# Kernel optimization log

Measured on AMD Instinct MI355X. Metric: run time of the kernel, lower is better.

## Reference

```python
import jax, jax.numpy as jnp
import numpy as np

N_NODES = 80000
N_EDGES = 1280000
NODE_DIM = 32
EDGE_DIM = 16
HIDDEN = 64
N_HIDDEN_LAYERS = 3  # layer_count - 1
NUM_GRAPHS = 256


def setup_inputs() -> dict:
    key = jax.random.key(0)
    ks = jax.random.split(key, 16)
    s = 0.05
    H = jax.random.normal(ks[0], (N_NODES, NODE_DIM), dtype=jnp.float32)
    Xe = jax.random.normal(ks[1], (N_EDGES, EDGE_DIM), dtype=jnp.float32)
    id_Xe = jax.random.randint(ks[2], (2, N_EDGES), 0, N_NODES, dtype=jnp.int32).astype(jnp.int64)
    batch_idx = jnp.sort(jax.random.randint(ks[3], (N_NODES,), 0, NUM_GRAPHS, dtype=jnp.int32)).astype(jnp.int64)
    # input layer: M: (node+edge)->hidden, U: (hidden+node)->hidden
    Mw0 = jax.random.normal(ks[4], (NODE_DIM + EDGE_DIM, HIDDEN), dtype=jnp.float32) * s
    Mb0 = jnp.zeros((HIDDEN,), dtype=jnp.float32)
    Uw0 = jax.random.normal(ks[5], (HIDDEN + NODE_DIM, HIDDEN), dtype=jnp.float32) * s
    Ub0 = jnp.zeros((HIDDEN,), dtype=jnp.float32)
    # hidden layers: M: (hidden+edge)->hidden, U: (2*hidden)->hidden (stacked)
    Mw_h = jax.random.normal(ks[6], (N_HIDDEN_LAYERS, HIDDEN + EDGE_DIM, HIDDEN), dtype=jnp.float32) * s
    Mb_h = jnp.zeros((N_HIDDEN_LAYERS, HIDDEN), dtype=jnp.float32)
    Uw_h = jax.random.normal(ks[7], (N_HIDDEN_LAYERS, 2 * HIDDEN, HIDDEN), dtype=jnp.float32) * s
    Ub_h = jnp.zeros((N_HIDDEN_LAYERS, HIDDEN), dtype=jnp.float32)
    # final linear head hidden -> 1
    Ww = jax.random.normal(ks[8], (HIDDEN, 1), dtype=jnp.float32) * s
    Wb = jnp.zeros((1,), dtype=jnp.float32)
    return {"H": H, "Xe": Xe, "id_Xe": id_Xe, "batch_idx": batch_idx,
            "Mw0": Mw0, "Mb0": Mb0, "Uw0": Uw0, "Ub0": Ub0,
            "Mw_h": Mw_h, "Mb_h": Mb_h, "Uw_h": Uw_h, "Ub_h": Ub_h,
            "Ww": Ww, "Wb": Wb}


def reference(H, Xe, id_Xe, batch_idx, Mw0, Mb0, Uw0, Ub0, Mw_h, Mb_h, Uw_h, Ub_h, Ww, Wb):
    n = H.shape[0]
    src = id_Xe[0]
    dst = id_Xe[1]

    def gnn_layer(h, Mw, Mb, Uw, Ub):
        # message: gather source node features, concat edge features, MLP M
        m = jax.nn.relu(jnp.concatenate([h[src], Xe], axis=-1) @ Mw + Mb)  # [E, hidden]
        # scatter-sum to target nodes
        agg = jax.ops.segment_sum(m, dst, num_segments=n)  # [N, hidden]
        # update: concat node state with aggregated message, MLP U
        return jax.nn.relu(jnp.concatenate([h, agg], axis=-1) @ Uw + Ub)

    y = gnn_layer(H, Mw0, Mb0, Uw0, Ub0)
    for i in range(Mw_h.shape[0]):
        y = gnn_layer(y, Mw_h[i], Mb_h[i], Uw_h[i], Ub_h[i])

    pooled = jax.ops.segment_sum(y, batch_idx, num_segments=NUM_GRAPHS)  # [G, hidden]
    return pooled @ Ww + Wb  # [G, 1]
```

## Files before the change

kernel.cpp:

```cpp
#include <hip/hip_runtime.h>
#include <hip/hip_fp16.h>

#define HID 64

struct alignas(8)  H4 { __half2 a, b; };
struct alignas(16) H8 { __half2 h[4]; };

typedef _Float16 h2n __attribute__((ext_vector_type(2)));

__device__ inline float dot2f(__half2 a, __half2 b, float c) {
#if __has_builtin(__builtin_amdgcn_fdot2)
    h2n an, bn;
    __builtin_memcpy(&an, &a, 4);
    __builtin_memcpy(&bn, &b, 4);
    return __builtin_amdgcn_fdot2(an, bn, c, false);
#else
    float2 af = __half22float2(a), bf = __half22float2(b);
    return c + af.x * bf.x + af.y * bf.y;
#endif
}

__global__ __launch_bounds__(256) void deg_count(const int* __restrict__ dst,
                                                 int* __restrict__ deg, int E) {
    int e = blockIdx.x * 256 + threadIdx.x;
    if (e < E) atomicAdd(&deg[dst[e]], 1);
}

__global__ __launch_bounds__(256) void scan1(const int* __restrict__ deg,
                                             int* __restrict__ rowptr,
                                             int* __restrict__ bsums, int N) {
    __shared__ int s[256];
    const int t = threadIdx.x;
    const int base = blockIdx.x * 2048 + t * 8;
    int v[8], tot = 0;
    #pragma unroll
    for (int i = 0; i < 8; i++) {
        int x = (base + i < N) ? deg[base + i] : 0;
        v[i] = tot; tot += x;
    }
    s[t] = tot; __syncthreads();
    for (int off = 1; off < 256; off <<= 1) {
        int a = (t >= off) ? s[t - off] : 0;
        __syncthreads(); s[t] += a; __syncthreads();
    }
    const int texcl = s[t] - tot;
    #pragma unroll
    for (int i = 0; i < 8; i++)
        if (base + i < N) rowptr[base + i] = texcl + v[i];
    if (t == 255) bsums[blockIdx.x] = s[255];
}

__global__ void scan2(int* bsums, int NB) {
    if (blockIdx.x == 0 && threadIdx.x == 0) {
        int run = 0;
        for (int i = 0; i < NB; i++) { int x = bsums[i]; bsums[i] = run; run += x; }
    }
}

__global__ __launch_bounds__(256) void scan3(int* __restrict__ rowptr,
                                             const int* __restrict__ bsums,
                                             int N, int E) {
    int idx = blockIdx.x * 256 + threadIdx.x;
    if (idx < N) rowptr[idx] += bsums[idx >> 11];
    if (idx == 0) rowptr[N] = E;
}

__global__ __launch_bounds__(256) void permute_k(
    const int* __restrict__ src, const int* __restrict__ dst,
    const int* __restrict__ rowptr, int* __restrict__ cursor,
    const float* __restrict__ Xe, __half* __restrict__ Xes,
    unsigned* __restrict__ pks, int E)
{
    int e = blockIdx.x * 256 + threadIdx.x;
    if (e >= E) return;
    int d = dst[e];
    int pos = rowptr[d] + atomicAdd(&cursor[d], 1);
    pks[pos] = ((unsigned)src[e] << 5) | (unsigned)(d & 31);
    const float4* xi = (const float4*)&Xe[(size_t)e * 16];
    float4 x0 = xi[0], x1 = xi[1], x2 = xi[2], x3 = xi[3];
    H8 h0, h1;
    h0.h[0] = __float22half2_rn(make_float2(x0.x, x0.y));
    h0.h[1] = __float22half2_rn(make_float2(x0.z, x0.w));
    h0.h[2] = __float22half2_rn(make_float2(x1.x, x1.y));
    h0.h[3] = __float22half2_rn(make_float2(x1.z, x1.w));
    h1.h[0] = __float22half2_rn(make_float2(x2.x, x2.y));
    h1.h[1] = __float22half2_rn(make_float2(x2.z, x2.w));
    h1.h[2] = __float22half2_rn(make_float2(x3.x, x3.y));
    h1.h[3] = __float22half2_rn(make_float2(x3.z, x3.w));
    H8* xo = (H8*)&Xes[(size_t)pos * 16];
    xo[0] = h0; xo[1] = h1;
}

template<int K1>
__global__ __launch_bounds__(256) void pm_dual(
    const float* __restrict__ Hn,
    const float* __restrict__ Wm, const float* __restrict__ bm,
    const float* __restrict__ Wu, const float* __restrict__ bu,
    __half* __restrict__ PMh, __half* __restrict__ Th, int N)
{
    constexpr int KP = K1 + 4;
    constexpr int P4 = K1 / 4;
    __shared__ float Ws[K1 * 128];
    __shared__ float Xs[32 * KP];

    const int tid = threadIdx.x;
    for (int i = tid; i < K1 * 32; i += 256) {
        const int row = i >> 5, c4 = i & 31;
        float4 v = (c4 < 16) ? *(const float4*)&Wm[row * 64 + c4 * 4]
                             : *(const float4*)&Wu[row * 64 + (c4 - 16) * 4];
        *(float4*)&Ws[row * 128 + c4 * 4] = v;
    }
    const int nbase = blockIdx.x * 32;
    for (int i = tid; i < 32 * P4; i += 256) {
        const int nl = i / P4, part = i % P4;
        const int n = nbase + nl;
        if (n < N)
            *(float4*)&Xs[nl * KP + part * 4] =
                *(const float4*)&Hn[(size_t)n * K1 + part * 4];
    }
    __syncthreads();

    const int c0 = (tid & 31) * 4;
    const int n0 = (tid >> 5) * 4;
    const float4 bv = (c0 < 64) ? *(const float4*)&bm[c0]
                                : *(const float4*)&bu[c0 - 64];

    float4 acc[4];
    #pragma unroll
    for (int i = 0; i < 4; i++) acc[i] = bv;

    #pragma unroll 4
    for (int k = 0; k < K1; k += 4) {
        const float4 w0 = *(const float4*)&Ws[(k + 0) * 128 + c0];
        const float4 w1 = *(const float4*)&Ws[(k + 1) * 128 + c0];
        const float4 w2 = *(const float4*)&Ws[(k + 2) * 128 + c0];
        const float4 w3 = *(const float4*)&Ws[(k + 3) * 128 + c0];
        #pragma unroll
        for (int ni = 0; ni < 4; ni++) {
            const float4 xv = *(const float4*)&Xs[(n0 + ni) * KP + k];
            acc[ni].x += xv.x * w0.x + xv.y * w1.x + xv.z * w2.x + xv.w * w3.x;
            acc[ni].y += xv.x * w0.y + xv.y * w1.y + xv.z * w2.y + xv.w * w3.y;
            acc[ni].z += xv.x * w0.z + xv.y * w1.z + xv.z * w2.z + xv.w * w3.z;
            acc[ni].w += xv.x * w0.w + xv.y * w1.w + xv.z * w2.w + xv.w * w3.w;
        }
    }

    #pragma unroll
    for (int ni = 0; ni < 4; ni++) {
        const int n = nbase + n0 + ni;
        if (n < N) {
            H4 o;
            o.a = __float22half2_rn(make_float2(acc[ni].x, acc[ni].y));
            o.b = __float22half2_rn(make_float2(acc[ni].z, acc[ni].w));
            if (c0 < 64) *(H4*)&PMh[(size_t)n * 64 + c0]      = o;
            else         *(H4*)&Th [(size_t)n * 64 + c0 - 64] = o;
        }
    }
}

__global__ __launch_bounds__(256) void edge_fused(
    const __half*   __restrict__ PMh,
    const __half*   __restrict__ Th,
    const __half*   __restrict__ Xes,
    const unsigned* __restrict__ pks,
    const int*      __restrict__ rowptr,
    const float*    __restrict__ Mwb,
    const float*    __restrict__ Uwb,
    float*          __restrict__ Yout,
    int N)
{
    constexpr int AGP = HID + 4;
    __shared__ float aggs[32 * AGP];

    const int tid  = threadIdx.x;
    const int wv   = tid >> 6;
    const int lane = tid & 63;
    const int c0   = (lane & 15) * 4;
    const int g    = lane >> 4;

    __half2 wh[8][4];
    #pragma unroll
    for (int p = 0; p < 8; p++)
        #pragma unroll
        for (int j = 0; j < 4; j++)
            wh[p][j] = __float22half2_rn(make_float2(Mwb[(2 * p) * 64 + c0 + j],
                                                     Mwb[(2 * p + 1) * 64 + c0 + j]));

    for (int i = tid; i < 32 * AGP; i += 256) aggs[i] = 0.f;

    const int nbase  = blockIdx.x * 32;
    const int nend   = (nbase + 32 < N) ? nbase + 32 : N;
    const int estart = rowptr[nbase];
    const int eend   = rowptr[nend];
    __syncthreads();

    int pc = estart + wv * 16;
    unsigned pk_c[4], pk_n[4], pk_n2[4];
    H4 ph_c[4], ph_n[4];
    H8 xh_c[4][2], xh_n[4][2];

    if (pc < eend) {
        #pragma unroll
        for (int s = 0; s < 4; s++) {
            const int pe = pc + g * 4 + s;
            pk_c[s] = pks[pe < eend ? pe : eend - 1];
        }
        if (pc + 64 < eend) {
            #pragma unroll
            for (int s = 0; s < 4; s++) {
                const int pe = pc + 64 + g * 4 + s;
                pk_n[s] = pks[pe < eend ? pe : eend - 1];
            }
        }
        #pragma unroll
        for (int s = 0; s < 4; s++) {
            const int pe  = pc + g * 4 + s;
            const int pcl = pe < eend ? pe : eend - 1;
            ph_c[s] = *(const H4*)&PMh[(size_t)(pk_c[s] >> 5) * 64 + c0];
            const H8* xr = (const H8*)&Xes[(size_t)pcl * 16];
            xh_c[s][0] = xr[0]; xh_c[s][1] = xr[1];
        }
    }

    for (; pc < eend; pc += 64) {
        const int pn  = pc + 64;
        const int pn2 = pc + 128;

        if (pn < eend) {
            #pragma unroll
            for (int s = 0; s < 4; s++) {
                const int pe  = pn + g * 4 + s;
                const int pcl = pe < eend ? pe : eend - 1;
                ph_n[s] = *(const H4*)&PMh[(size_t)(pk_n[s] >> 5) * 64 + c0];
                const H8* xr = (const H8*)&Xes[(size_t)pcl * 16];
                xh_n[s][0] = xr[0]; xh_n[s][1] = xr[1];
            }
        }
        if (pn2 < eend) {
            #pragma unroll
            for (int s = 0; s < 4; s++) {
                const int pe = pn2 + g * 4 + s;
                pk_n2[s] = pks[pe < eend ? pe : eend - 1];
            }
        }

        int ld_prev = -1;
        float4 racc = make_float4(0.f, 0.f, 0.f, 0.f);
        #pragma unroll
        for (int s = 0; s < 4; s++) {
            const bool valid = (pc + g * 4 + s) < eend;
            const float2 pl = __half22float2(ph_c[s].a);
            const float2 pu = __half22float2(ph_c[s].b);
            float a0 = pl.x, a1 = pl.y, a2 = pu.x, a3 = pu.y;
            #pragma unroll
            for (int p = 0; p < 8; p++) {
                const __half2 xv = xh_c[s][p >> 2].h[p & 3];
                a0 = dot2f(xv, wh[p][0], a0);
                a1 = dot2f(xv, wh[p][1], a1);
                a2 = dot2f(xv, wh[p][2], a2);
                a3 = dot2f(xv, wh[p][3], a3);
            }
            float4 v;
            v.x = fmaxf(a0, 0.f); v.y = fmaxf(a1, 0.f);
            v.z = fmaxf(a2, 0.f); v.w = fmaxf(a3, 0.f);
            const int ld = valid ? (int)(pk_c[s] & 31u) : -1;
            if (ld == ld_prev) {
                racc.x += v.x; racc.y += v.y; racc.z += v.z; racc.w += v.w;
            } else {
                if (ld_prev >= 0) {
                    float* a = &aggs[ld_prev * AGP + c0];
                    atomicAdd(a + 0, racc.x); atomicAdd(a + 1, racc.y);
                    atomicAdd(a + 2, racc.z); atomicAdd(a + 3, racc.w);
                }
                racc = v; ld_prev = ld;
            }
        }
        if (ld_prev >= 0) {
            float* a = &aggs[ld_prev * AGP + c0];
            atomicAdd(a + 0, racc.x); atomicAdd(a + 1, racc.y);
            atomicAdd(a + 2, racc.z); atomicAdd(a + 3, racc.w);
        }

        #pragma unroll
        for (int s = 0; s < 4; s++) {
            pk_c[s] = pk_n[s]; pk_n[s] = pk_n2[s];
            ph_c[s] = ph_n[s];
            xh_c[s][0] = xh_n[s][0]; xh_c[s][1] = xh_n[s][1];
        }
    }

    __syncthreads();

    {
        const int c0t = (tid & 15) * 4;
        const int r0  = tid >> 4;
        const int r1  = r0 + 16;
        const int n0g = nbase + r0, n1g = nbase + r1;
        float4 acc0 = make_float4(0.f, 0.f, 0.f, 0.f);
        float4 acc1 = make_float4(0.f, 0.f, 0.f, 0.f);
        if (n0g < N) {
            H4 th = *(const H4*)&Th[(size_t)n0g * 64 + c0t];
            float2 lo = __half22float2(th.a), hi = __half22float2(th.b);
            acc0 = make_float4(lo.x, lo.y, hi.x, hi.y);
        }
        if (n1g < N) {
            H4 th = *(const H4*)&Th[(size_t)n1g * 64 + c0t];
            float2 lo = __half22float2(th.a), hi = __half22float2(th.b);
            acc1 = make_float4(lo.x, lo.y, hi.x, hi.y);
        }
        #pragma unroll 4
        for (int k = 0; k < 64; k += 4) {
            const float4 w0 = *(const float4*)&Uwb[(k + 0) * 64 + c0t];
            const float4 w1 = *(const float4*)&Uwb[(k + 1) * 64 + c0t];
            const float4 w2 = *(const float4*)&Uwb[(k + 2) * 64 + c0t];
            const float4 w3 = *(const float4*)&Uwb[(k + 3) * 64 + c0t];
            const float4 x0 = *(const float4*)&aggs[r0 * AGP + k];
            const float4 x1 = *(const float4*)&aggs[r1 * AGP + k];
            acc0.x += x0.x * w0.x + x0.y * w1.x + x0.z * w2.x + x0.w * w3.x;
            acc0.y += x0.x * w0.y + x0.y * w1.y + x0.z * w2.y + x0.w * w3.y;
            acc0.z += x0.x * w0.z + x0.y * w1.z + x0.z * w2.z + x0.w * w3.z;
            acc0.w += x0.x * w0.w + x0.y * w1.w + x0.z * w2.w + x0.w * w3.w;
            acc1.x += x1.x * w0.x + x1.y * w1.x + x1.z * w2.x + x1.w * w3.x;
            acc1.y += x1.x * w0.y + x1.y * w1.y + x1.z * w2.y + x1.w * w3.y;
            acc1.z += x1.x * w0.z + x1.y * w1.z + x1.z * w2.z + x1.w * w3.z;
            acc1.w += x1.x * w0.w + x1.y * w1.w + x1.z * w2.w + x1.w * w3.w;
        }
        if (n0g < N) {
            float4 o;
            o.x = fmaxf(acc0.x, 0.f); o.y = fmaxf(acc0.y, 0.f);
            o.z = fmaxf(acc0.z, 0.f); o.w = fmaxf(acc0.w, 0.f);
            *(float4*)&Yout[(size_t)n0g * HID + c0t] = o;
        }
        if (n1g < N) {
            float4 o;
            o.x = fmaxf(acc1.x, 0.f); o.y = fmaxf(acc1.y, 0.f);
            o.z = fmaxf(acc1.z, 0.f); o.w = fmaxf(acc1.w, 0.f);
            *(float4*)&Yout[(size_t)n1g * HID + c0t] = o;
        }
    }
}

__global__ __launch_bounds__(256) void pool_head(
    const float* __restrict__ Y, const int* __restrict__ bidx,
    const float* __restrict__ Ww, const float* __restrict__ Wb,
    float* __restrict__ out, int N)
{
    const int g = blockIdx.x;
    int a = 0, b = N;
    while (a < b) { int m = (a + b) >> 1; if (bidx[m] < g) a = m + 1; else b = m; }
    const int lo = a;
    b = N;
    while (a < b) { int m = (a + b) >> 1; if (bidx[m] < g + 1) a = m + 1; else b = m; }
    const int hi = a;

    const int tid = threadIdx.x;
    const int c4 = tid & 15, nl = tid >> 4;
    float4 s = make_float4(0.f, 0.f, 0.f, 0.f);
    for (int n = lo + nl; n < hi; n += 16) {
        const float4 v = *(const float4*)&Y[(size_t)n * HID + c4 * 4];
        s.x += v.x; s.y += v.y; s.z += v.z; s.w += v.w;
    }
    __shared__ float red[16 * 68];
    *(float4*)&red[nl * 68 + c4 * 4] = s;
    __syncthreads();
    if (tid < 64) {
        float t = 0.f;
        #pragma unroll
        for (int r = 0; r < 16; r++) t += red[r * 68 + tid];
        t *= Ww[tid];
        #pragma unroll
        for (int off = 32; off; off >>= 1) t += __shfl_down(t, off);
        if (tid == 0) out[g] = t + Wb[0];
    }
}

extern "C" void kernel_launch(void* const* d_in, const int* in_sizes, int n_in,
                              void* d_out, int out_size, void* d_ws, size_t ws_size,
                              hipStream_t stream) {
    const float* H    = (const float*)d_in[0];
    const float* Xe   = (const float*)d_in[1];
    const int*   ids  = (const int*)d_in[2];
    const int*   bidx = (const int*)d_in[3];
    const float* Mw0  = (const float*)d_in[4];
    const float* Mb0  = (const float*)d_in[5];
    const float* Uw0  = (const float*)d_in[6];
    const float* Ub0  = (const float*)d_in[7];
    const float* MwH  = (const float*)d_in[8];
    const float* MbH  = (const float*)d_in[9];
    const float* UwH  = (const float*)d_in[10];
    const float* UbH  = (const float*)d_in[11];
    const float* Ww   = (const float*)d_in[12];
    const float* Wb   = (const float*)d_in[13];
    float* out = (float*)d_out;

    const int N = in_sizes[0] / 32;
    const int E = in_sizes[1] / 16;
    const int* src = ids;
    const int* dst = ids + E;

    float*  hbuf = (float*)d_ws;
    __half* PMh  = (__half*)(hbuf + (size_t)N * HID);
    __half* Th   = PMh + (size_t)N * HID;
    __half* Xes  = Th  + (size_t)N * HID;
    unsigned* pks = (unsigned*)(Xes + (size_t)E * 16);
    int* rowptr  = (int*)(pks + E);
    int* deg     = rowptr + (N + 1);
    int* bsums   = deg + N;

    const int NB = (N + 2047) / 2048;
    const int eblocks = (E + 255) / 256;
    const int ntile   = (N + 31) / 32;

    hipMemsetAsync(deg, 0, (size_t)N * sizeof(int), stream);
    deg_count<<<eblocks, 256, 0, stream>>>(dst, deg, E);
    scan1<<<NB, 256, 0, stream>>>(deg, rowptr, bsums, N);
    scan2<<<1, 64, 0, stream>>>(bsums, NB);
    scan3<<<(N + 255) / 256, 256, 0, stream>>>(rowptr, bsums, N, E);
    hipMemsetAsync(deg, 0, (size_t)N * sizeof(int), stream);
    permute_k<<<eblocks, 256, 0, stream>>>(src, dst, rowptr, deg,
                                           Xe, Xes, pks, E);

    pm_dual<32><<<ntile, 256, 0, stream>>>(H, Mw0, Mb0, Uw0, Ub0, PMh, Th, N);
    edge_fused<<<ntile, 256, 0, stream>>>(PMh, Th, Xes, pks, rowptr,
                                          Mw0 + 32 * HID, Uw0 + 32 * HID, hbuf, N);

    for (int l = 0; l < 3; l++) {
        const float* Mw = MwH + (size_t)l * 80 * HID;
        const float* Uw = UwH + (size_t)l * 128 * HID;
        pm_dual<64><<<ntile, 256, 0, stream>>>(hbuf, Mw, MbH + (size_t)l * HID,
                                               Uw, UbH + (size_t)l * HID, PMh, Th, N);
        edge_fused<<<ntile, 256, 0, stream>>>(PMh, Th, Xes, pks, rowptr,
                                              Mw + 64 * HID, Uw + 64 * HID, hbuf, N);
    }

    pool_head<<<256, 256, 0, stream>>>(hbuf, bidx, Ww, Wb, out, N);
}
```

Measured before the change: 967.2 us.

## Fuse next layer's node projection into edge kernel epilogue with ping-pong buffers

The edge_fused kernel is templated so that, for the first three layers, its epilogue keeps the ReLU'd node state in shared memory. It then directly computes the next layer's message and update projections (the former pm_dual work), writing them as fp16 into alternating buffers. This drops three pm_dual launches and the fp32 round trip of the hidden state through global memory. In exchange the epilogue needs an extra block sync, and each block does more register and compute work. The final layer writes fp32 output into a region that aliases the no-longer-used ping buffers.

```diff
diff --git a/kernel.cpp b/kernel.cpp
--- a/kernel.cpp
+++ b/kernel.cpp
@@ -158,6 +158,7 @@
     }
 }
 
+template<bool FUSE>
 __global__ __launch_bounds__(256) void edge_fused(
     const __half*   __restrict__ PMh,
     const __half*   __restrict__ Th,
@@ -166,6 +167,12 @@
     const int*      __restrict__ rowptr,
     const float*    __restrict__ Mwb,
     const float*    __restrict__ Uwb,
+    const float*    __restrict__ MwN,
+    const float*    __restrict__ MbN,
+    const float*    __restrict__ UwN,
+    const float*    __restrict__ UbN,
+    __half*         __restrict__ PMo,
+    __half*         __restrict__ Tho,
     float*          __restrict__ Yout,
     int N)
 {
@@ -291,51 +298,100 @@
 
     __syncthreads();
 
-    {
-        const int c0t = (tid & 15) * 4;
-        const int r0  = tid >> 4;
-        const int r1  = r0 + 16;
-        const int n0g = nbase + r0, n1g = nbase + r1;
-        float4 acc0 = make_float4(0.f, 0.f, 0.f, 0.f);
-        float4 acc1 = make_float4(0.f, 0.f, 0.f, 0.f);
-        if (n0g < N) {
-            H4 th = *(const H4*)&Th[(size_t)n0g * 64 + c0t];
-            float2 lo = __half22float2(th.a), hi = __half22float2(th.b);
-            acc0 = make_float4(lo.x, lo.y, hi.x, hi.y);
-        }
-        if (n1g < N) {
-            H4 th = *(const H4*)&Th[(size_t)n1g * 64 + c0t];
-            float2 lo = __half22float2(th.a), hi = __half22float2(th.b);
-            acc1 = make_float4(lo.x, lo.y, hi.x, hi.y);
-        }
+    const int c0t = (tid & 15) * 4;
+    const int r0  = tid >> 4;
+    const int r1  = r0 + 16;
+    const int n0g = nbase + r0, n1g = nbase + r1;
+    float4 acc0 = make_float4(0.f, 0.f, 0.f, 0.f);
+    float4 acc1 = make_float4(0.f, 0.f, 0.f, 0.f);
+    if (n0g < N) {
+        H4 th = *(const H4*)&Th[(size_t)n0g * 64 + c0t];
+        float2 lo = __half22float2(th.a), hi = __half22float2(th.b);
+        acc0 = make_float4(lo.x, lo.y, hi.x, hi.y);
+    }
+    if (n1g < N) {
+        H4 th = *(const H4*)&Th[(size_t)n1g * 64 + c0t];
+        float2 lo = __half22float2(th.a), hi = __half22float2(th.b);
+        acc1 = make_float4(lo.x, lo.y, hi.x, hi.y);
+    }
+    #pragma unroll 4
+    for (int k = 0; k < 64; k += 4) {
+        const float4 w0 = *(const float4*)&Uwb[(k + 0) * 64 + c0t];
+        const float4 w1 = *(const float4*)&Uwb[(k + 1) * 64 + c0t];
+        const float4 w2 = *(const float4*)&Uwb[(k + 2) * 64 + c0t];
+        const float4 w3 = *(const float4*)&Uwb[(k + 3) * 64 + c0t];
+        const float4 x0 = *(const float4*)&aggs[r0 * AGP + k];
+        const float4 x1 = *(const float4*)&aggs[r1 * AGP + k];
+        acc0.x += x0.x * w0.x + x0.y * w1.x + x0.z * w2.x + x0.w * w3.x;
+        acc0.y += x0.x * w0.y + x0.y * w1.y + x0.z * w2.y + x0.w * w3.y;
+        acc0.z += x0.x * w0.z + x0.y * w1.z + x0.z * w2.z + x0.w * w3.z;
+        acc0.w += x0.x * w0.w + x0.y * w1.w + x0.z * w2.w + x0.w * w3.w;
+        acc1.x += x1.x * w0.x + x1.y * w1.x + x1.z * w2.x + x1.w * w3.x;
+        acc1.y += x1.x * w0.y + x1.y * w1.y + x1.z * w2.y + x1.w * w3.y;
+        acc1.z += x1.x * w0.z + x1.y * w1.z + x1.z * w2.z + x1.w * w3.z;
+        acc1.w += x1.x * w0.w + x1.y * w1.w + x1.z * w2.w + x1.w * w3.w;
+    }
+    float4 y0, y1;
+    y0.x = fmaxf(acc0.x, 0.f); y0.y = fmaxf(acc0.y, 0.f);
+    y0.z = fmaxf(acc0.z, 0.f); y0.w = fmaxf(acc0.w, 0.f);
+    y1.x = fmaxf(acc1.x, 0.f); y1.y = fmaxf(acc1.y, 0.f);
+    y1.z = fmaxf(acc1.z, 0.f); y1.w = fmaxf(acc1.w, 0.f);
+
+    if (!FUSE) {
+        if (n0g < N) *(float4*)&Yout[(size_t)n0g * HID + c0t] = y0;
+        if (n1g < N) *(float4*)&Yout[(size_t)n1g * HID + c0t] = y1;
+    } else {
+        __syncthreads();
+        *(float4*)&aggs[r0 * AGP + c0t] = y0;
+        *(float4*)&aggs[r1 * AGP + c0t] = y1;
+        __syncthreads();
+
+        const int c2  = (tid & 31) * 4;
+        const int nn0 = (tid >> 5) * 4;
+        const bool isM = (c2 < 64);
+        const float* Wn = isM ? MwN : UwN;
+        const float* bn = isM ? MbN : UbN;
+        const int cc = isM ? c2 : c2 - 64;
+        const float4 bv = *(const float4*)&bn[cc];
+        float4 p0 = bv, p1 = bv, p2 = bv, p3 = bv;
         #pragma unroll 4
         for (int k = 0; k < 64; k += 4) {
-            const float4 w0 = *(const float4*)&Uwb[(k + 0) * 64 + c0t];
-            const float4 w1 = *(const float4*)&Uwb[(k + 1) * 64 + c0t];
-            const float4 w2 = *(const float4*)&Uwb[(k + 2) * 64 + c0t];
-            const float4 w3 = *(const float4*)&Uwb[(k + 3) * 64 + c0t];
-            const float4 x0 = *(const float4*)&aggs[r0 * AGP + k];
-            const float4 x1 = *(const float4*)&aggs[r1 * AGP + k];
-            acc0.x += x0.x * w0.x + x0.y * w1.x + x0.z * w2.x + x0.w * w3.x;
-            acc0.y += x0.x * w0.y + x0.y * w1.y + x0.z * w2.y + x0.w * w3.y;
-            acc0.z += x0.x * w0.z + x0.y * w1.z + x0.z * w2.z + x0.w * w3.z;
-            acc0.w += x0.x * w0.w + x0.y * w1.w + x0.z * w2.w + x0.w * w3.w;
-            acc1.x += x1.x * w0.x + x1.y * w1.x + x1.z * w2.x + x1.w * w3.x;
-            acc1.y += x1.x * w0.y + x1.y * w1.y + x1.z * w2.y + x1.w * w3.y;
-            acc1.z += x1.x * w0.z + x1.y * w1.z + x1.z * w2.z + x1.w * w3.z;
-            acc1.w += x1.x * w0.w + x1.y * w1.w + x1.z * w2.w + x1.w * w3.w;
-        }
-        if (n0g < N) {
-            float4 o;
-            o.x = fmaxf(acc0.x, 0.f); o.y = fmaxf(acc0.y, 0.f);
-            o.z = fmaxf(acc0.z, 0.f); o.w = fmaxf(acc0.w, 0.f);
-            *(float4*)&Yout[(size_t)n0g * HID + c0t] = o;
-        }
-        if (n1g < N) {
-            float4 o;
-            o.x = fmaxf(acc1.x, 0.f); o.y = fmaxf(acc1.y, 0.f);
-            o.z = fmaxf(acc1.z, 0.f); o.w = fmaxf(acc1.w, 0.f);
-            *(float4*)&Yout[(size_t)n1g * HID + c0t] = o;
+            const float4 w0 = *(const float4*)&Wn[(k + 0) * 64 + cc];
+            const float4 w1 = *(const float4*)&Wn[(k + 1) * 64 + cc];
+            const float4 w2 = *(const float4*)&Wn[(k + 2) * 64 + cc];
+            const float4 w3 = *(const float4*)&Wn[(k + 3) * 64 + cc];
+            const float4 x0 = *(const float4*)&aggs[(nn0 + 0) * AGP + k];
+            const float4 x1 = *(const float4*)&aggs[(nn0 + 1) * AGP + k];
+            const float4 x2 = *(const float4*)&aggs[(nn0 + 2) * AGP + k];
+            const float4 x3 = *(const float4*)&aggs[(nn0 + 3) * AGP + k];
+            p0.x += x0.x * w0.x + x0.y * w1.x + x0.z * w2.x + x0.w * w3.x;
+            p0.y += x0.x * w0.y + x0.y * w1.y + x0.z * w2.y + x0.w * w3.y;
+            p0.z += x0.x * w0.z + x0.y * w1.z + x0.z * w2.z + x0.w * w3.z;
+            p0.w += x0.x * w0.w + x0.y * w1.w + x0.z * w2.w + x0.w * w3.w;
+            p1.x += x1.x * w0.x + x1.y * w1.x + x1.z * w2.x + x1.w * w3.x;
+            p1.y += x1.x * w0.y + x1.y * w1.y + x1.z * w2.y + x1.w * w3.y;
+            p1.z += x1.x * w0.z + x1.y * w1.z + x1.z * w2.z + x1.w * w3.z;
+            p1.w += x1.x * w0.w + x1.y * w1.w + x1.z * w2.w + x1.w * w3.w;
+            p2.x += x2.x * w0.x + x2.y * w1.x + x2.z * w2.x + x2.w * w3.x;
+            p2.y += x2.x * w0.y + x2.y * w1.y + x2.z * w2.y + x2.w * w3.y;
+            p2.z += x2.x * w0.z + x2.y * w1.z + x2.z * w2.z + x2.w * w3.z;
+            p2.w += x2.x * w0.w + x2.y * w1.w + x2.z * w2.w + x2.w * w3.w;
+            p3.x += x3.x * w0.x + x3.y * w1.x + x3.z * w2.x + x3.w * w3.x;
+            p3.y += x3.x * w0.y + x3.y * w1.y + x3.z * w2.y + x3.w * w3.y;
+            p3.z += x3.x * w0.z + x3.y * w1.z + x3.z * w2.z + x3.w * w3.z;
+            p3.w += x3.x * w0.w + x3.y * w1.w + x3.z * w2.w + x3.w * w3.w;
+        }
+        float4 pr[4] = {p0, p1, p2, p3};
+        #pragma unroll
+        for (int ni = 0; ni < 4; ni++) {
+            const int n = nbase + nn0 + ni;
+            if (n < N) {
+                H4 o;
+                o.a = __float22half2_rn(make_float2(pr[ni].x, pr[ni].y));
+                o.b = __float22half2_rn(make_float2(pr[ni].z, pr[ni].w));
+                if (isM) *(H4*)&PMo[(size_t)n * 64 + cc] = o;
+                else     *(H4*)&Tho[(size_t)n * 64 + cc] = o;
+            }
         }
     }
 }
@@ -398,10 +454,12 @@
     const int* src = ids;
     const int* dst = ids + E;
 
-    float*  hbuf = (float*)d_ws;
-    __half* PMh  = (__half*)(hbuf + (size_t)N * HID);
-    __half* Th   = PMh + (size_t)N * HID;
-    __half* Xes  = Th  + (size_t)N * HID;
+    __half* PMa  = (__half*)d_ws;
+    __half* Tha  = PMa + (size_t)N * HID;
+    __half* PMb  = Tha + (size_t)N * HID;
+    __half* Thb  = PMb + (size_t)N * HID;
+    float*  yfin = (float*)d_ws;
+    __half* Xes  = Thb + (size_t)N * HID;
     unsigned* pks = (unsigned*)(Xes + (size_t)E * 16);
     int* rowptr  = (int*)(pks + E);
     int* deg     = rowptr + (N + 1);
@@ -420,18 +478,34 @@
     permute_k<<<eblocks, 256, 0, stream>>>(src, dst, rowptr, deg,
                                            Xe, Xes, pks, E);
 
-    pm_dual<32><<<ntile, 256, 0, stream>>>(H, Mw0, Mb0, Uw0, Ub0, PMh, Th, N);
-    edge_fused<<<ntile, 256, 0, stream>>>(PMh, Th, Xes, pks, rowptr,
-                                          Mw0 + 32 * HID, Uw0 + 32 * HID, hbuf, N);
-
-    for (int l = 0; l < 3; l++) {
-        const float* Mw = MwH + (size_t)l * 80 * HID;
-        const float* Uw = UwH + (size_t)l * 128 * HID;
-        pm_dual<64><<<ntile, 256, 0, stream>>>(hbuf, Mw, MbH + (size_t)l * HID,
-                                               Uw, UbH + (size_t)l * HID, PMh, Th, N);
-        edge_fused<<<ntile, 256, 0, stream>>>(PMh, Th, Xes, pks, rowptr,
-                                              Mw + 64 * HID, Uw + 64 * HID, hbuf, N);
-    }
-
-    pool_head<<<256, 256, 0, stream>>>(hbuf, bidx, Ww, Wb, out, N);
-}
+    const float* MwH0 = MwH;                 const float* UwH0 = UwH;
+    const float* MwH1 = MwH + 80 * HID;      const float* UwH1 = UwH + 128 * HID;
+    const float* MwH2 = MwH + 2 * 80 * HID;  const float* UwH2 = UwH + 2 * 128 * HID;
+
+    pm_dual<32><<<ntile, 256, 0, stream>>>(H, Mw0, Mb0, Uw0, Ub0, PMa, Tha, N);
+    edge_fused<true><<<ntile, 256, 0, stream>>>(
+        PMa, Tha, Xes, pks, rowptr,
+        Mw0 + 32 * HID, Uw0 + 32 * HID,
+        MwH0, MbH, UwH0, UbH,
+        PMb, Thb, nullptr, N);
+
+    edge_fused<true><<<ntile, 256, 0, stream>>>(
+        PMb, Thb, Xes, pks, rowptr,
+        MwH0 + 64 * HID, UwH0 + 64 * HID,
+        MwH1, MbH + HID, UwH1, UbH + HID,
+        PMa, Tha, nullptr, N);
+
+    edge_fused<true><<<ntile, 256, 0, stream>>>(
+        PMa, Tha, Xes, pks, rowptr,
+        MwH1 + 64 * HID, UwH1 + 64 * HID,
+        MwH2, MbH + 2 * HID, UwH2, UbH + 2 * HID,
+        PMb, Thb, nullptr, N);
+
+    edge_fused<false><<<ntile, 256, 0, stream>>>(
+        PMb, Thb, Xes, pks, rowptr,
+        MwH2 + 64 * HID, UwH2 + 64 * HID,
+        nullptr, nullptr, nullptr, nullptr,
+        nullptr, nullptr, yfin, N);
+
+    pool_head<<<256, 256, 0, stream>>>(yfin, bidx, Ww, Wb, out, N);
+}
```

New measurement: 914.4 us. 1.06x faster.
